# Performance work log

Measured on AMD Instinct MI355X. Metric: run time of the kernel, lower is better.

The kernel has to match this reference:

```python
import jax, jax.numpy as jnp
import numpy as np

HIDDEN = 1024
HEADS = 16
HEAD = HIDDEN // HEADS


def setup_inputs() -> dict:
    key = jax.random.key(0)
    k1, k2, k3 = jax.random.split(key, 3)
    scale = 1.0 / np.sqrt(HIDDEN)
    return {
        "hidden_states": jax.random.normal(k1, (2, 2048, HIDDEN), dtype=jnp.float32),
        "w_qkv": jax.random.normal(k2, (HIDDEN, 3 * HIDDEN), dtype=jnp.float32) * scale,
        "b_qkv": jnp.zeros((3 * HIDDEN,), dtype=jnp.float32),
        "w_dense": jax.random.normal(k3, (HIDDEN, HIDDEN), dtype=jnp.float32) * scale,
        "b_dense": jnp.zeros((HIDDEN,), dtype=jnp.float32),
    }


def reference(hidden_states, w_qkv, b_qkv, w_dense, b_dense):
    B, S, H = hidden_states.shape
    qkv = hidden_states @ w_qkv + b_qkv                      # [B,S,3H]
    qkv = qkv.reshape(B, S, HEADS, 3 * HEAD).transpose(0, 2, 1, 3)  # [B,h,S,3d]
    q, k, v = jnp.split(qkv, 3, axis=-1)                      # each [B,h,S,d]
    scores = jnp.einsum("bhqd,bhkd->bhqk", q, k) / np.sqrt(HEAD)
    probs = jax.nn.softmax(scores, axis=-1)                   # [B,h,S,S]
    ctx = jnp.einsum("bhqk,bhkd->bhqd", probs, v)             # [B,h,S,d]
    ctx = ctx.transpose(0, 2, 1, 3).reshape(B, S, H)
    return ctx @ w_dense + b_dense
```

## Files before the change

### kernel.cpp

```cpp
#include <hip/hip_runtime.h>

#define L2E 1.44269504088896f

typedef unsigned short u16;
typedef __attribute__((ext_vector_type(8))) short bf16x8;
typedef __attribute__((ext_vector_type(4))) float f32x4;
typedef __attribute__((ext_vector_type(16))) float f32x16;

__device__ __forceinline__ u16 f2bf(float x) {
  union { float f; unsigned u; } a; a.f = x;
  return (u16)((a.u + 0x7fffu + ((a.u >> 16) & 1u)) >> 16);
}

__device__ __forceinline__ unsigned cvtpk(float lo, float hi) {
  unsigned r;
  asm("v_cvt_pk_bf16_f32 %0, %1, %2" : "=v"(r) : "v"(lo), "v"(hi));
  return r;
}

__device__ __forceinline__ float fexp2(float x) {
  float r;
  asm("v_exp_f32 %0, %1" : "=v"(r) : "v"(x));
  return r;
}

__device__ __forceinline__ void gll16(const u16* g, u16* lds) {
  __builtin_amdgcn_global_load_lds(
      (const __attribute__((address_space(1))) unsigned int*)g,
      (__attribute__((address_space(3))) unsigned int*)lds, 16, 0, 0);
}

__global__ __launch_bounds__(256) void cvt_bf16(const float* __restrict__ in,
                                                u16* __restrict__ out, int n4) {
  int i = blockIdx.x * 256 + threadIdx.x;
  int stride = gridDim.x * 256;
  for (; i < n4; i += stride) {
    float4 v = reinterpret_cast<const float4*>(in)[i];
    ushort4 o;
    o.x = f2bf(v.x); o.y = f2bf(v.y); o.z = f2bf(v.z); o.w = f2bf(v.w);
    reinterpret_cast<ushort4*>(out)[i] = o;
  }
}

__global__ __launch_bounds__(256) void transpose_cvt(const float* __restrict__ in,
                                                     u16* __restrict__ out,
                                                     int K, int N) {
  __shared__ float tile[32][33];
  int n0 = blockIdx.x * 32, k0 = blockIdx.y * 32;
  int tx = threadIdx.x & 31, ty = threadIdx.x >> 5;
  for (int r = ty; r < 32; r += 8)
    tile[r][tx] = in[(k0 + r) * N + n0 + tx];
  __syncthreads();
  for (int r = ty; r < 32; r += 8)
    out[(n0 + r) * K + k0 + tx] = f2bf(tile[tx][r]);
}

__global__ __launch_bounds__(256) void gemm_qkv(
    const u16* __restrict__ A, const u16* __restrict__ Bt,
    const float* __restrict__ bias,
    u16* __restrict__ Qo, u16* __restrict__ Ko, u16* __restrict__ Vt) {
  __shared__ __attribute__((aligned(16))) u16 As[2][128 * 64];
  __shared__ __attribute__((aligned(16))) u16 Bs[2][128 * 64];
  const int t = threadIdx.x, w = t >> 6, l = t & 63;
  const int m0 = blockIdx.y * 128, n0 = blockIdx.x * 128;
  const int lr = l & 15, lk = l >> 4;
  const int wr = (w >> 1) * 64, wc = (w & 1) * 64;
  const int sr = l >> 3;
  const int sch = (l & 7) ^ sr;
  f32x4 acc[4][4] = {};

#define QSTAGE(bi, k0)                                                        \
  do {                                                                        \
    _Pragma("unroll")                                                         \
    for (int j = 0; j < 4; ++j) {                                             \
      const int rb = w * 32 + j * 8;                                          \
      gll16(A + (size_t)(m0 + rb + sr) * 1024 + (k0) + sch * 8,               \
            &As[bi][rb * 64]);                                                \
      gll16(Bt + (size_t)(n0 + rb + sr) * 1024 + (k0) + sch * 8,              \
            &Bs[bi][rb * 64]);                                                \
    }                                                                         \
  } while (0)

  QSTAGE(0, 0);
  for (int kt = 0; kt < 16; ++kt) {
    const int buf = kt & 1;
    if (kt < 15) {
      QSTAGE(buf ^ 1, (kt + 1) * 64);
      asm volatile("s_waitcnt vmcnt(8)" ::: "memory");
    } else {
      asm volatile("s_waitcnt vmcnt(0)" ::: "memory");
    }
    __builtin_amdgcn_s_barrier();
    const u16* Asb = As[buf];
    const u16* Bsb = Bs[buf];
#pragma unroll
    for (int kk = 0; kk < 2; ++kk) {
      bf16x8 a[4], b[4];
#pragma unroll
      for (int mf = 0; mf < 4; ++mf) {
        const int row = wr + mf * 16 + lr;
        const int ch = (kk * 4 + lk) ^ (row & 7);
        a[mf] = *reinterpret_cast<const bf16x8*>(&Asb[row * 64 + ch * 8]);
      }
#pragma unroll
      for (int nf = 0; nf < 4; ++nf) {
        const int row = wc + nf * 16 + lr;
        const int ch = (kk * 4 + lk) ^ (row & 7);
        b[nf] = *reinterpret_cast<const bf16x8*>(&Bsb[row * 64 + ch * 8]);
      }
#pragma unroll
      for (int mf = 0; mf < 4; ++mf)
#pragma unroll
        for (int nf = 0; nf < 4; ++nf)
          acc[mf][nf] = __builtin_amdgcn_mfma_f32_16x16x32_bf16(a[mf], b[nf],
                                                                acc[mf][nf], 0, 0, 0);
    }
    asm volatile("" ::: "memory");
    __builtin_amdgcn_s_barrier();
  }
#undef QSTAGE

  const float QSC = 0.125f * L2E;
#pragma unroll
  for (int mf = 0; mf < 4; ++mf)
#pragma unroll
    for (int nf = 0; nf < 4; ++nf) {
      const int gc = n0 + wc + nf * 16 + lr;
      const int h = gc / 192, j = gc - h * 192;
      const int part = j >> 6, d = j & 63;
      const float bv = bias[gc];
      const int gr0 = m0 + wr + mf * 16 + lk * 4;
      const int b_ = gr0 >> 11, s0 = gr0 & 2047;
      if (part == 2) {
        const int s0p = (s0 & ~0xC) | ((s0 & 4) << 1) | ((s0 & 8) >> 1);
        union { ushort4 s; unsigned u[2]; } pk;
        pk.u[0] = cvtpk(acc[mf][nf][0] + bv, acc[mf][nf][1] + bv);
        pk.u[1] = cvtpk(acc[mf][nf][2] + bv, acc[mf][nf][3] + bv);
        *reinterpret_cast<ushort4*>(
            &Vt[((size_t)(b_ * 16 + h) * 64 + d) * 2048 + s0p]) = pk.s;
      } else if (part == 0) {
#pragma unroll
        for (int r = 0; r < 4; ++r)
          Qo[((size_t)(b_ * 16 + h) * 2048 + s0 + r) * 64 + d] =
              f2bf((acc[mf][nf][r] + bv) * QSC);
      } else {
#pragma unroll
        for (int r = 0; r < 4; ++r)
          Ko[((size_t)(b_ * 16 + h) * 2048 + s0 + r) * 64 + d] =
              f2bf(acc[mf][nf][r] + bv);
      }
    }
}

__global__ __launch_bounds__(256) void attn2(
    const u16* __restrict__ Q, const u16* __restrict__ K,
    const u16* __restrict__ Vt, u16* __restrict__ ctx) {
  __shared__ __attribute__((aligned(16))) u16 Ks[2][64 * 64];
  __shared__ __attribute__((aligned(16))) u16 Vs[2][64 * 64];
  const int t = threadIdx.x;
  const int w = t >> 6, l = t & 63;
  const int lq = l & 31, hi = l >> 5;
  const int bid = blockIdx.x;
  const int wg = (bid & 7) * 64 + (bid >> 3);
  const int bh = wg >> 4, qt = wg & 15;
  const int b = bh >> 4, h = bh & 15;
  const u16* Qp = Q + (size_t)bh * (2048 * 64);
  const u16* Kp = K + (size_t)bh * (2048 * 64);
  const u16* Vp = Vt + (size_t)bh * (64 * 2048);
  const int q0w = qt * 128 + w * 32;

  const int srow = w * 16 + (l >> 3);
  const int sch = (l & 7) ^ ((l >> 3) & 7);

  bf16x8 qf[4];
#pragma unroll
  for (int i = 0; i < 4; ++i)
    qf[i] = *reinterpret_cast<const bf16x8*>(
        &Qp[(size_t)(q0w + lq) * 64 + i * 16 + hi * 8]);

  bf16x8 ones;
#pragma unroll
  for (int j = 0; j < 8; ++j) ones[j] = (short)0x3F80;

  f32x16 o0 = {}, o1 = {}, osum = {};
  float mrun = -1e30f;

#define STG(bufi, kk0)                                                         \
  do {                                                                         \
    gll16(Kp + (size_t)((kk0) + srow) * 64 + sch * 8,                          \
          &Ks[bufi][(w * 16) * 64]);                                           \
    gll16(Kp + (size_t)((kk0) + srow + 8) * 64 + sch * 8,                      \
          &Ks[bufi][(w * 16 + 8) * 64]);                                       \
    gll16(Vp + (size_t)srow * 2048 + (kk0) + sch * 8,                          \
          &Vs[bufi][(w * 16) * 64]);                                           \
    gll16(Vp + (size_t)(srow + 8) * 2048 + (kk0) + sch * 8,                    \
          &Vs[bufi][(w * 16 + 8) * 64]);                                       \
  } while (0)

#define PVSTEP(pp, sub)                                                        \
  do {                                                                         \
    _Pragma("unroll")                                                          \
    for (int kb = 0; kb < 2; ++kb) {                                           \
      union { unsigned u[4]; bf16x8 v; } pu;                                   \
      pu.u[0] = cvtpk(pp[8 * kb + 0], pp[8 * kb + 1]);                         \
      pu.u[1] = cvtpk(pp[8 * kb + 2], pp[8 * kb + 3]);                         \
      pu.u[2] = cvtpk(pp[8 * kb + 4], pp[8 * kb + 5]);                         \
      pu.u[3] = cvtpk(pp[8 * kb + 6], pp[8 * kb + 7]);                         \
      const int ch = (((sub) * 4 + kb * 2 + hi) ^ (lq & 7)) * 8;               \
      bf16x8 v0 = *reinterpret_cast<const bf16x8*>(&VB[lq * 64 + ch]);         \
      o0 = __builtin_amdgcn_mfma_f32_32x32x16_bf16(v0, pu.v, o0, 0, 0, 0);     \
      bf16x8 v1 = *reinterpret_cast<const bf16x8*>(&VB[(32 + lq) * 64 + ch]);  \
      o1 = __builtin_amdgcn_mfma_f32_32x32x16_bf16(v1, pu.v, o1, 0, 0, 0);     \
      osum = __builtin_amdgcn_mfma_f32_32x32x16_bf16(ones, pu.v, osum, 0, 0, 0);\
    }                                                                          \
  } while (0)

  STG(0, 0);

#pragma unroll 2
  for (int kt = 0; kt < 32; ++kt) {
    const int buf = kt & 1;
    if (kt < 31) {
      STG(buf ^ 1, (kt + 1) * 64);
      asm volatile("s_waitcnt vmcnt(4)" ::: "memory");
    } else {
      asm volatile("s_waitcnt vmcnt(0)" ::: "memory");
    }
    __builtin_amdgcn_s_barrier();
    const u16* KB = Ks[buf];
    const u16* VB = Vs[buf];

    f32x16 s0 = {}, s1 = {};
#pragma unroll
    for (int i = 0; i < 4; ++i) {
      const int sl = ((2 * i + hi) ^ (lq & 7)) * 8;
      bf16x8 k0f = *reinterpret_cast<const bf16x8*>(&KB[lq * 64 + sl]);
      s0 = __builtin_amdgcn_mfma_f32_32x32x16_bf16(k0f, qf[i], s0, 0, 0, 0);
      bf16x8 k1f = *reinterpret_cast<const bf16x8*>(&KB[(32 + lq) * 64 + sl]);
      s1 = __builtin_amdgcn_mfma_f32_32x32x16_bf16(k1f, qf[i], s1, 0, 0, 0);
    }

    float mx[8];
#pragma unroll
    for (int r = 0; r < 8; ++r)
      mx[r] = fmaxf(fmaxf(s0[r], s0[r + 8]), fmaxf(s1[r], s1[r + 8]));
#pragma unroll
    for (int r = 0; r < 4; ++r) mx[r] = fmaxf(mx[r], mx[r + 4]);
    float tm = fmaxf(fmaxf(mx[0], mx[1]), fmaxf(mx[2], mx[3]));
    tm = fmaxf(tm, __shfl_xor(tm, 32));

    if (!__all(tm - mrun <= 8.0f)) {
      float mnew = fmaxf(mrun, tm);
      float al = fexp2(mrun - mnew);
      mrun = mnew;
#pragma unroll
      for (int r = 0; r < 16; ++r) { o0[r] *= al; o1[r] *= al; }
      osum[0] *= al;
    }

    float p0[16], p1[16];
#pragma unroll
    for (int r = 0; r < 16; ++r) p0[r] = fexp2(s0[r] - mrun);
#pragma unroll
    for (int r = 0; r < 16; ++r) p1[r] = fexp2(s1[r] - mrun);

    PVSTEP(p0, 0);
    PVSTEP(p1, 1);

    asm volatile("" ::: "memory");
    __builtin_amdgcn_s_barrier();
  }
#undef STG
#undef PVSTEP

  const float inv = 1.0f / osum[0];
  u16* cp = ctx + ((size_t)(b * 2048 + q0w + lq) * 1024 + h * 64);
#pragma unroll
  for (int a = 0; a < 4; ++a) {
    const int d = 8 * a + 4 * hi;
    union { ushort4 s; unsigned u[2]; } pk;
    pk.u[0] = cvtpk(o0[4 * a + 0] * inv, o0[4 * a + 1] * inv);
    pk.u[1] = cvtpk(o0[4 * a + 2] * inv, o0[4 * a + 3] * inv);
    *reinterpret_cast<ushort4*>(cp + d) = pk.s;
    pk.u[0] = cvtpk(o1[4 * a + 0] * inv, o1[4 * a + 1] * inv);
    pk.u[1] = cvtpk(o1[4 * a + 2] * inv, o1[4 * a + 3] * inv);
    *reinterpret_cast<ushort4*>(cp + 32 + d) = pk.s;
  }
}

__global__ __launch_bounds__(256) void gemm_dense(
    const u16* __restrict__ A, const u16* __restrict__ Bt,
    const float* __restrict__ bias, float* __restrict__ out) {
  __shared__ __attribute__((aligned(16))) u16 As[2][128 * 64];
  __shared__ __attribute__((aligned(16))) u16 Bs[2][64 * 64];
  const int t = threadIdx.x, w = t >> 6, l = t & 63;
  const int m0 = blockIdx.y * 128, n0 = blockIdx.x * 64;
  const int lr = l & 15, lk = l >> 4;
  const int wr = (w >> 1) * 64, wc = (w & 1) * 32;
  const int sr = l >> 3;
  const int sch = (l & 7) ^ sr;
  f32x4 acc[4][2] = {};

#define DSTAGE(bi, k0)                                                        \
  do {                                                                        \
    _Pragma("unroll")                                                         \
    for (int j = 0; j < 4; ++j) {                                             \
      const int rb = w * 32 + j * 8;                                          \
      gll16(A + (size_t)(m0 + rb + sr) * 1024 + (k0) + sch * 8,               \
            &As[bi][rb * 64]);                                                \
    }                                                                         \
    _Pragma("unroll")                                                         \
    for (int j = 0; j < 2; ++j) {                                             \
      const int rb = w * 16 + j * 8;                                          \
      gll16(Bt + (size_t)(n0 + rb + sr) * 1024 + (k0) + sch * 8,              \
            &Bs[bi][rb * 64]);                                                \
    }                                                                         \
  } while (0)

  DSTAGE(0, 0);
  for (int kt = 0; kt < 16; ++kt) {
    const int buf = kt & 1;
    if (kt < 15) {
      DSTAGE(buf ^ 1, (kt + 1) * 64);
      asm volatile("s_waitcnt vmcnt(6)" ::: "memory");
    } else {
      asm volatile("s_waitcnt vmcnt(0)" ::: "memory");
    }
    __builtin_amdgcn_s_barrier();
    const u16* Asb = As[buf];
    const u16* Bsb = Bs[buf];
#pragma unroll
    for (int kk = 0; kk < 2; ++kk) {
      bf16x8 a[4], b[2];
#pragma unroll
      for (int mf = 0; mf < 4; ++mf) {
        const int row = wr + mf * 16 + lr;
        const int ch = (kk * 4 + lk) ^ (row & 7);
        a[mf] = *reinterpret_cast<const bf16x8*>(&Asb[row * 64 + ch * 8]);
      }
#pragma unroll
      for (int nf = 0; nf < 2; ++nf) {
        const int row = wc + nf * 16 + lr;
        const int ch = (kk * 4 + lk) ^ (row & 7);
        b[nf] = *reinterpret_cast<const bf16x8*>(&Bsb[row * 64 + ch * 8]);
      }
#pragma unroll
      for (int mf = 0; mf < 4; ++mf)
#pragma unroll
        for (int nf = 0; nf < 2; ++nf)
          acc[mf][nf] = __builtin_amdgcn_mfma_f32_16x16x32_bf16(a[mf], b[nf],
                                                                acc[mf][nf], 0, 0, 0);
    }
    asm volatile("" ::: "memory");
    __builtin_amdgcn_s_barrier();
  }
#undef DSTAGE

#pragma unroll
  for (int mf = 0; mf < 4; ++mf)
#pragma unroll
    for (int nf = 0; nf < 2; ++nf)
#pragma unroll
      for (int r = 0; r < 4; ++r) {
        int gr = m0 + wr + mf * 16 + lk * 4 + r;
        int gc = n0 + wc + nf * 16 + lr;
        out[(size_t)gr * 1024 + gc] = acc[mf][nf][r] + bias[gc];
      }
}

extern "C" void kernel_launch(void* const* d_in, const int* in_sizes, int n_in,
                              void* d_out, int out_size, void* d_ws, size_t ws_size,
                              hipStream_t stream) {
  const float* hs = (const float*)d_in[0];
  const float* w_qkv = (const float*)d_in[1];
  const float* b_qkv = (const float*)d_in[2];
  const float* w_dense = (const float*)d_in[3];
  const float* b_dense = (const float*)d_in[4];
  float* out = (float*)d_out;

  char* ws = (char*)d_ws;
  u16* hsb = (u16*)(ws);
  u16* wqkvT = (u16*)(ws + (8ll << 20));
  u16* wdT = (u16*)(ws + (14ll << 20));
  u16* Qb = (u16*)(ws + (16ll << 20));
  u16* Kb = (u16*)(ws + (24ll << 20));
  u16* Vtb = (u16*)(ws + (32ll << 20));
  u16* ctx = (u16*)(ws + (40ll << 20));

  cvt_bf16<<<dim3(2048), dim3(256), 0, stream>>>(hs, hsb, (4096 * 1024) / 4);
  transpose_cvt<<<dim3(96, 32), dim3(256), 0, stream>>>(w_qkv, wqkvT, 1024, 3072);
  transpose_cvt<<<dim3(32, 32), dim3(256), 0, stream>>>(w_dense, wdT, 1024, 1024);
  gemm_qkv<<<dim3(24, 32), dim3(256), 0, stream>>>(hsb, wqkvT, b_qkv, Qb, Kb, Vtb);
  attn2<<<dim3(512), dim3(256), 0, stream>>>(Qb, Kb, Vtb, ctx);
  gemm_dense<<<dim3(16, 32), dim3(256), 0, stream>>>(ctx, wdT, b_dense, out);
}
```

Baseline: 199.6 us.

## Fuse prep kernels into one launch and stage two K/V tiles per barrier in attention

Merges the hidden-state conversion and both weight transpose-convert kernels into a single prep launch, removing two kernel launches. In the attention kernel, each pipeline stage now loads two 64-key K/V tiles into LDS, which halves the number of barrier rounds per key sweep and issues more loads in flight before each wait. LDS use doubles to 64KB per block, which may reduce occupancy.

```diff
diff --git a/kernel.cpp b/kernel.cpp
--- a/kernel.cpp
+++ b/kernel.cpp
@@ -30,24 +30,33 @@
       (__attribute__((address_space(3))) unsigned int*)lds, 16, 0, 0);
 }
 
-__global__ __launch_bounds__(256) void cvt_bf16(const float* __restrict__ in,
-                                                u16* __restrict__ out, int n4) {
-  int i = blockIdx.x * 256 + threadIdx.x;
-  int stride = gridDim.x * 256;
-  for (; i < n4; i += stride) {
-    float4 v = reinterpret_cast<const float4*>(in)[i];
-    ushort4 o;
-    o.x = f2bf(v.x); o.y = f2bf(v.y); o.z = f2bf(v.z); o.w = f2bf(v.w);
-    reinterpret_cast<ushort4*>(out)[i] = o;
-  }
-}
-
-__global__ __launch_bounds__(256) void transpose_cvt(const float* __restrict__ in,
-                                                     u16* __restrict__ out,
-                                                     int K, int N) {
+__global__ __launch_bounds__(256) void prep(
+    const float* __restrict__ hs, u16* __restrict__ hsb,
+    const float* __restrict__ wq, u16* __restrict__ wqT,
+    const float* __restrict__ wd, u16* __restrict__ wdT) {
   __shared__ float tile[32][33];
-  int n0 = blockIdx.x * 32, k0 = blockIdx.y * 32;
-  int tx = threadIdx.x & 31, ty = threadIdx.x >> 5;
+  const int bid = blockIdx.x;
+  if (bid < 1024) {
+    int i = bid * 256 + threadIdx.x;
+    for (; i < (4096 * 1024 / 4); i += 1024 * 256) {
+      float4 v = reinterpret_cast<const float4*>(hs)[i];
+      ushort4 o;
+      o.x = f2bf(v.x); o.y = f2bf(v.y); o.z = f2bf(v.z); o.w = f2bf(v.w);
+      reinterpret_cast<ushort4*>(hsb)[i] = o;
+    }
+    return;
+  }
+  const float* in; u16* out; int K, N, n0, k0;
+  if (bid < 1024 + 3072) {
+    const int idx = bid - 1024;
+    in = wq; out = wqT; K = 1024; N = 3072;
+    n0 = (idx % 96) * 32; k0 = (idx / 96) * 32;
+  } else {
+    const int idx = bid - 4096;
+    in = wd; out = wdT; K = 1024; N = 1024;
+    n0 = (idx & 31) * 32; k0 = (idx >> 5) * 32;
+  }
+  const int tx = threadIdx.x & 31, ty = threadIdx.x >> 5;
   for (int r = ty; r < 32; r += 8)
     tile[r][tx] = in[(k0 + r) * N + n0 + tx];
   __syncthreads();
@@ -155,8 +164,8 @@
 __global__ __launch_bounds__(256) void attn2(
     const u16* __restrict__ Q, const u16* __restrict__ K,
     const u16* __restrict__ Vt, u16* __restrict__ ctx) {
-  __shared__ __attribute__((aligned(16))) u16 Ks[2][64 * 64];
-  __shared__ __attribute__((aligned(16))) u16 Vs[2][64 * 64];
+  __shared__ __attribute__((aligned(16))) u16 Ks[2][2][64 * 64];
+  __shared__ __attribute__((aligned(16))) u16 Vs[2][2][64 * 64];
   const int t = threadIdx.x;
   const int w = t >> 6, l = t & 63;
   const int lq = l & 31, hi = l >> 5;
@@ -185,17 +194,20 @@
   f32x16 o0 = {}, o1 = {}, osum = {};
   float mrun = -1e30f;
 
-#define STG(bufi, kk0)                                                         \
+#define STG1(bufi, sub, kk0)                                                   \
   do {                                                                         \
     gll16(Kp + (size_t)((kk0) + srow) * 64 + sch * 8,                          \
-          &Ks[bufi][(w * 16) * 64]);                                           \
+          &Ks[bufi][sub][(w * 16) * 64]);                                      \
     gll16(Kp + (size_t)((kk0) + srow + 8) * 64 + sch * 8,                      \
-          &Ks[bufi][(w * 16 + 8) * 64]);                                       \
+          &Ks[bufi][sub][(w * 16 + 8) * 64]);                                  \
     gll16(Vp + (size_t)srow * 2048 + (kk0) + sch * 8,                          \
-          &Vs[bufi][(w * 16) * 64]);                                           \
+          &Vs[bufi][sub][(w * 16) * 64]);                                      \
     gll16(Vp + (size_t)(srow + 8) * 2048 + (kk0) + sch * 8,                    \
-          &Vs[bufi][(w * 16 + 8) * 64]);                                       \
+          &Vs[bufi][sub][(w * 16 + 8) * 64]);                                  \
   } while (0)
+
+#define STGPAIR(bufi, kk0)                                                     \
+  do { STG1(bufi, 0, kk0); STG1(bufi, 1, (kk0) + 64); } while (0)
 
 #define PVSTEP(pp, sub)                                                        \
   do {                                                                         \
@@ -215,62 +227,66 @@
     }                                                                          \
   } while (0)
 
-  STG(0, 0);
-
-#pragma unroll 2
-  for (int kt = 0; kt < 32; ++kt) {
-    const int buf = kt & 1;
-    if (kt < 31) {
-      STG(buf ^ 1, (kt + 1) * 64);
-      asm volatile("s_waitcnt vmcnt(4)" ::: "memory");
+  STGPAIR(0, 0);
+
+  for (int kt2 = 0; kt2 < 16; ++kt2) {
+    const int buf = kt2 & 1;
+    if (kt2 < 15) {
+      STGPAIR(buf ^ 1, (kt2 + 1) * 128);
+      asm volatile("s_waitcnt vmcnt(8)" ::: "memory");
     } else {
       asm volatile("s_waitcnt vmcnt(0)" ::: "memory");
     }
     __builtin_amdgcn_s_barrier();
-    const u16* KB = Ks[buf];
-    const u16* VB = Vs[buf];
-
-    f32x16 s0 = {}, s1 = {};
-#pragma unroll
-    for (int i = 0; i < 4; ++i) {
-      const int sl = ((2 * i + hi) ^ (lq & 7)) * 8;
-      bf16x8 k0f = *reinterpret_cast<const bf16x8*>(&KB[lq * 64 + sl]);
-      s0 = __builtin_amdgcn_mfma_f32_32x32x16_bf16(k0f, qf[i], s0, 0, 0, 0);
-      bf16x8 k1f = *reinterpret_cast<const bf16x8*>(&KB[(32 + lq) * 64 + sl]);
-      s1 = __builtin_amdgcn_mfma_f32_32x32x16_bf16(k1f, qf[i], s1, 0, 0, 0);
-    }
-
-    float mx[8];
-#pragma unroll
-    for (int r = 0; r < 8; ++r)
-      mx[r] = fmaxf(fmaxf(s0[r], s0[r + 8]), fmaxf(s1[r], s1[r + 8]));
-#pragma unroll
-    for (int r = 0; r < 4; ++r) mx[r] = fmaxf(mx[r], mx[r + 4]);
-    float tm = fmaxf(fmaxf(mx[0], mx[1]), fmaxf(mx[2], mx[3]));
-    tm = fmaxf(tm, __shfl_xor(tm, 32));
-
-    if (!__all(tm - mrun <= 8.0f)) {
-      float mnew = fmaxf(mrun, tm);
-      float al = fexp2(mrun - mnew);
-      mrun = mnew;
-#pragma unroll
-      for (int r = 0; r < 16; ++r) { o0[r] *= al; o1[r] *= al; }
-      osum[0] *= al;
-    }
-
-    float p0[16], p1[16];
-#pragma unroll
-    for (int r = 0; r < 16; ++r) p0[r] = fexp2(s0[r] - mrun);
-#pragma unroll
-    for (int r = 0; r < 16; ++r) p1[r] = fexp2(s1[r] - mrun);
-
-    PVSTEP(p0, 0);
-    PVSTEP(p1, 1);
+
+#pragma unroll
+    for (int sub = 0; sub < 2; ++sub) {
+      const u16* KB = Ks[buf][sub];
+      const u16* VB = Vs[buf][sub];
+
+      f32x16 s0 = {}, s1 = {};
+#pragma unroll
+      for (int i = 0; i < 4; ++i) {
+        const int sl = ((2 * i + hi) ^ (lq & 7)) * 8;
+        bf16x8 k0f = *reinterpret_cast<const bf16x8*>(&KB[lq * 64 + sl]);
+        s0 = __builtin_amdgcn_mfma_f32_32x32x16_bf16(k0f, qf[i], s0, 0, 0, 0);
+        bf16x8 k1f = *reinterpret_cast<const bf16x8*>(&KB[(32 + lq) * 64 + sl]);
+        s1 = __builtin_amdgcn_mfma_f32_32x32x16_bf16(k1f, qf[i], s1, 0, 0, 0);
+      }
+
+      float mx[8];
+#pragma unroll
+      for (int r = 0; r < 8; ++r)
+        mx[r] = fmaxf(fmaxf(s0[r], s0[r + 8]), fmaxf(s1[r], s1[r + 8]));
+#pragma unroll
+      for (int r = 0; r < 4; ++r) mx[r] = fmaxf(mx[r], mx[r + 4]);
+      float tm = fmaxf(fmaxf(mx[0], mx[1]), fmaxf(mx[2], mx[3]));
+      tm = fmaxf(tm, __shfl_xor(tm, 32));
+
+      if (!__all(tm - mrun <= 8.0f)) {
+        float mnew = fmaxf(mrun, tm);
+        float al = fexp2(mrun - mnew);
+        mrun = mnew;
+#pragma unroll
+        for (int r = 0; r < 16; ++r) { o0[r] *= al; o1[r] *= al; }
+        osum[0] *= al;
+      }
+
+      float p0[16], p1[16];
+#pragma unroll
+      for (int r = 0; r < 16; ++r) p0[r] = fexp2(s0[r] - mrun);
+#pragma unroll
+      for (int r = 0; r < 16; ++r) p1[r] = fexp2(s1[r] - mrun);
+
+      PVSTEP(p0, 0);
+      PVSTEP(p1, 1);
+    }
 
     asm volatile("" ::: "memory");
     __builtin_amdgcn_s_barrier();
   }
-#undef STG
+#undef STG1
+#undef STGPAIR
 #undef PVSTEP
 
   const float inv = 1.0f / osum[0];
@@ -387,9 +403,7 @@
   u16* Vtb = (u16*)(ws + (32ll << 20));
   u16* ctx = (u16*)(ws + (40ll << 20));
 
-  cvt_bf16<<<dim3(2048), dim3(256), 0, stream>>>(hs, hsb, (4096 * 1024) / 4);
-  transpose_cvt<<<dim3(96, 32), dim3(256), 0, stream>>>(w_qkv, wqkvT, 1024, 3072);
-  transpose_cvt<<<dim3(32, 32), dim3(256), 0, stream>>>(w_dense, wdT, 1024, 1024);
+  prep<<<dim3(5120), dim3(256), 0, stream>>>(hs, hsb, w_qkv, wqkvT, w_dense, wdT);
   gemm_qkv<<<dim3(24, 32), dim3(256), 0, stream>>>(hsb, wqkvT, b_qkv, Qb, Kb, Vtb);
   attn2<<<dim3(512), dim3(256), 0, stream>>>(Qb, Kb, Vtb, ctx);
   gemm_dense<<<dim3(16, 32), dim3(256), 0, stream>>>(ctx, wdT, b_dense, out);
```

Result: faster. 191.8 us (-3.9%).
